# Kernel tuning notes

Measured on AMD Instinct MI355X. Metric: run time of the kernel, lower is better.

The kernel has to match this reference:

```python
import jax, jax.numpy as jnp
import numpy as np

OUT_SIZE = 7
SPATIAL_SCALE = 0.0625
SAMPLE_NUM = 2


def setup_inputs() -> dict:
    key = jax.random.key(0)
    k1, k2, k3, k4, k5, k6 = jax.random.split(key, 6)
    N, C, H, W = 4, 256, 96, 96
    K = 1024
    features = jax.random.normal(k1, (N, C, H, W), dtype=jnp.float32)
    img_h, img_w = H / SPATIAL_SCALE, W / SPATIAL_SCALE
    batch_idx = jax.random.randint(k2, (K,), 0, N).astype(jnp.float32)
    x1 = jax.random.uniform(k3, (K,)) * (img_w - 320.0)
    y1 = jax.random.uniform(k4, (K,)) * (img_h - 320.0)
    x2 = x1 + 16.0 + jax.random.uniform(k5, (K,)) * 300.0
    y2 = y1 + 16.0 + jax.random.uniform(k6, (K,)) * 300.0
    rois = jnp.stack([batch_idx, x1, y1, x2, y2], axis=1).astype(jnp.float32)
    return {"features": features, "rois": rois}


def _sample_coords(start, bin_size):
    # start, bin_size: [K]; returns [K, OUT_SIZE*SAMPLE_NUM] sample-point coords
    g = jnp.arange(OUT_SIZE * SAMPLE_NUM, dtype=jnp.float32)
    bin_idx = jnp.floor(g / SAMPLE_NUM)
    sub = g - bin_idx * SAMPLE_NUM
    offs = bin_idx + (sub + 0.5) / SAMPLE_NUM
    return start[:, None] + bin_size[:, None] * offs[None, :]


def _interp_1d(coord, size):
    # coord: [K, G] sample coords along one axis of a map of length `size`.
    valid = (coord >= -1.0) & (coord <= jnp.float32(size))
    c = jnp.clip(coord, 0.0, jnp.float32(size - 1))
    lo = jnp.floor(c)
    hi = jnp.minimum(lo + 1.0, jnp.float32(size - 1))
    frac = c - lo  # weight of hi; (1-frac) weight of lo
    return lo.astype(jnp.int32), hi.astype(jnp.int32), frac, valid


def roi_align(features, rois):
    N, C, H, W = features.shape
    b = rois[:, 0].astype(jnp.int32)
    x1, y1, x2, y2 = (rois[:, i] * SPATIAL_SCALE for i in (1, 2, 3, 4))
    roi_w = jnp.maximum(x2 - x1, 1.0)
    roi_h = jnp.maximum(y2 - y1, 1.0)
    bin_w = roi_w / OUT_SIZE
    bin_h = roi_h / OUT_SIZE

    ys = _sample_coords(y1, bin_h)  # [K, G]
    xs = _sample_coords(x1, bin_w)  # [K, G]
    ylo, yhi, fy, vy = _interp_1d(ys, H)
    xlo, xhi, fx, vx = _interp_1d(xs, W)

    bb = b[:, None, None]

    def gather(yi, xi):
        # -> [K, G, G, C]
        return features[bb, :, yi[:, :, None], xi[:, None, :]]

    wy_lo, wy_hi = (1.0 - fy), fy
    wx_lo, wx_hi = (1.0 - fx), fx

    def w2(wy, wx):
        return (wy[:, :, None] * wx[:, None, :])[..., None]

    val = (gather(ylo, xlo) * w2(wy_lo, wx_lo)
           + gather(ylo, xhi) * w2(wy_lo, wx_hi)
           + gather(yhi, xlo) * w2(wy_hi, wx_lo)
           + gather(yhi, xhi) * w2(wy_hi, wx_hi))
    mask = (vy[:, :, None] & vx[:, None, :])[..., None]
    val = jnp.where(mask, val, 0.0)

    K = rois.shape[0]
    G = OUT_SIZE * SAMPLE_NUM
    val = val.reshape(K, OUT_SIZE, SAMPLE_NUM, OUT_SIZE, SAMPLE_NUM, C)
    out = val.mean(axis=(2, 4))          # average the sample points per bin
    return jnp.transpose(out, (0, 3, 1, 2))  # [K, C, out, out]


def reference(features, rois):
    return roi_align(features, rois)
```

## Files before the change

### kernel.cpp

```cpp
#include <hip/hip_runtime.h>

#define CCH   256
#define FH    96
#define FW    96
#define HW    (FH*FW)
#define SCALE 0.0625f

#define HROWS 21
#define PSTR  28
#define PLANE (HROWS*PSTR)
#define WCH   32

__global__ __launch_bounds__(256, 8)
void roialign_kernel(const float* __restrict__ feat,
                     const float* __restrict__ rois,
                     float* __restrict__ out)
{
    __shared__ __align__(16) float win[4 * PLANE];
    __shared__ int   s_lo[2][14];
    __shared__ float s_wl[2][14], s_wh[2][14];

    const int k    = blockIdx.x >> 1;
    const int half = blockIdx.x & 1;
    const int tid  = threadIdx.x;
    const int w    = tid >> 6;
    const int ll   = tid & 63;

    const float x1 = rois[k*5+1] * SCALE;
    const float y1 = rois[k*5+2] * SCALE;
    const float x2 = rois[k*5+3] * SCALE;
    const float y2 = rois[k*5+4] * SCALE;
    const int   b  = (int)rois[k*5+0];
    const float binw = fmaxf(x2 - x1, 1.0f) * (1.0f/7.0f);
    const float binh = fmaxf(y2 - y1, 1.0f) * (1.0f/7.0f);

    if (tid < 28) {
        const int   axis  = (tid >= 14) ? 1 : 0;
        const int   g     = axis ? tid - 14 : tid;
        const float start = axis ? x1 : y1;
        const float bsz   = axis ? binw : binh;
        const float offs  = (float)(g >> 1) + 0.25f + 0.5f*(float)(g & 1);
        const float coord = start + bsz * offs;
        const bool  valid = (coord >= -1.0f) && (coord <= 96.0f);
        const float cc    = fminf(fmaxf(coord, 0.0f), 95.0f);
        const float lof   = floorf(cc);
        const float frac  = cc - lof;
        const float v     = valid ? 1.0f : 0.0f;
        s_lo[axis][g] = (int)lof;
        s_wl[axis][g] = (1.0f - frac) * v;
        s_wh[axis][g] = frac * v;
    }
    __syncthreads();

    const int row0 = s_lo[0][0];
    const int col0 = min(s_lo[1][0] & ~3, FW - 24);
    int hw_        = min(s_lo[0][13] + 1, FH-1) - row0 + 1;
    const int hwin = min(hw_, HROWS);
    const int nslot = hwin * 6;

    float* const wp = &win[w * PLANE];

    {
        const float4 z = make_float4(0.f, 0.f, 0.f, 0.f);
        #pragma unroll
        for (int j = 0; j < 3; ++j) {
            const int q = ll + 64*j;
            if (q < PLANE/4) *(float4*)&wp[q*4] = z;
        }
    }

    const bool active = ll < 49;
    const int  p  = active ? ll : 0;
    const int  oy = p / 7;
    const int  ox = p - oy*7;

    int   aL[4], aH[4];
    float w00[4], w01[4], w10[4], w11[4];
    #pragma unroll
    for (int sy = 0; sy < 2; ++sy) {
        const int   gy  = 2*oy + sy;
        const int   rlo = min(s_lo[0][gy] - row0,                 HROWS-1);
        const int   rhi = min(min(s_lo[0][gy]+1, FH-1) - row0,    HROWS-1);
        const float wyl = s_wl[0][gy], wyh = s_wh[0][gy];
        #pragma unroll
        for (int sx = 0; sx < 2; ++sx) {
            const int   gx  = 2*ox + sx;
            const int   clo = min(s_lo[1][gx] - col0, PSTR-2);
            const float wxl = s_wl[1][gx], wxh = s_wh[1][gx];
            const int   s   = sy*2 + sx;
            aL[s] = rlo*PSTR + clo;
            aH[s] = rhi*PSTR + clo;
            w00[s] = wyl*wxl*0.25f;  w01[s] = wyl*wxh*0.25f;
            w10[s] = wyh*wxl*0.25f;  w11[s] = wyh*wxh*0.25f;
        }
    }

    const int  sl1 = ll + 64;
    const int  r0  = ll  / 6, q0 = ll  - r0*6;
    const int  r1  = sl1 / 6, q1 = sl1 - r1*6;
    const bool L0  = ll  < nslot;
    const bool L1  = sl1 < nslot;
    const int  goff0 = min(row0 + r0, FH-1)*FW + col0 + q0*4;
    const int  goff1 = min(row0 + r1, FH-1)*FW + col0 + q1*4;
    const int  ld0   = min(r0, HROWS-1)*PSTR + q0*4;
    const int  ld1   = min(r1, HROWS-1)*PSTR + q1*4;

    const int    cb   = half*128 + w*WCH;
    const float* gch  = feat + (size_t)(b*CCH + cb) * HW;
    float*       outp = out  + ((size_t)k*CCH + cb)*49 + p;

    float4 st0, st1;
    if (L0) st0 = *(const float4*)(gch + goff0);
    if (L1) st1 = *(const float4*)(gch + goff1);

    for (int c = 0; c < WCH; ++c) {
        if (L0) *(float4*)&wp[ld0] = st0;
        if (L1) *(float4*)&wp[ld1] = st1;

        if (c + 1 < WCH) {
            const float* gn = gch + (size_t)(c+1)*HW;
            if (L0) st0 = *(const float4*)(gn + goff0);
            if (L1) st1 = *(const float4*)(gn + goff1);
        }

        if (active) {
            float acc = 0.0f;
            #pragma unroll
            for (int s = 0; s < 4; ++s) {
                acc += w00[s]*wp[aL[s]]   + w01[s]*wp[aL[s]+1]
                     + w10[s]*wp[aH[s]]   + w11[s]*wp[aH[s]+1];
            }
            outp[0] = acc;
        }
        outp += 49;
    }
}

extern "C" void kernel_launch(void* const* d_in, const int* in_sizes, int n_in,
                              void* d_out, int out_size, void* d_ws, size_t ws_size,
                              hipStream_t stream) {
    const float* feat = (const float*)d_in[0];
    const float* rois = (const float*)d_in[1];
    float*       outp = (float*)d_out;
    const int K = in_sizes[1] / 5;
    roialign_kernel<<<K*2, 256, 0, stream>>>(feat, rois, outp);
}
```

Before: 135.6 us.

## Apply y-interpolation while staging rows, making LDS hold per-sample-row vectors

Separates the bilinear interpolation: each loader thread reads the lo and hi feature rows for one y-sample and writes the y-blended row into shared memory. The compute threads then only perform the x-interpolation, with 8 LDS reads instead of 16 per output. The shared buffer becomes 14 sample rows instead of a 21-row window, at the cost of twice as many global loads per staged row, since adjacent samples' rows are fetched redundantly. Launch bounds occupancy hint is lowered from 8 to 6.

Measured after the change: 144.7 us. 6.7% more time.

```diff
diff --git a/kernel.cpp b/kernel.cpp
--- a/kernel.cpp
+++ b/kernel.cpp
@@ -6,19 +6,20 @@
 #define HW    (FH*FW)
 #define SCALE 0.0625f
 
-#define HROWS 21
-#define PSTR  28
-#define PLANE (HROWS*PSTR)
+#define G     14
+#define VSTR  28
+#define PLANE (G*VSTR)
 #define WCH   32
+#define NSLOT 84
 
-__global__ __launch_bounds__(256, 8)
+__global__ __launch_bounds__(256, 6)
 void roialign_kernel(const float* __restrict__ feat,
                      const float* __restrict__ rois,
                      float* __restrict__ out)
 {
-    __shared__ __align__(16) float win[4 * PLANE];
-    __shared__ int   s_lo[2][14];
-    __shared__ float s_wl[2][14], s_wh[2][14];
+    __shared__ __align__(16) float vbuf[4 * PLANE];
+    __shared__ int   s_lo[2][G];
+    __shared__ float s_wl[2][G], s_wh[2][G];
 
     const int k    = blockIdx.x >> 1;
     const int half = blockIdx.x & 1;
@@ -52,85 +53,81 @@
     }
     __syncthreads();
 
-    const int row0 = s_lo[0][0];
     const int col0 = min(s_lo[1][0] & ~3, FW - 24);
-    int hw_        = min(s_lo[0][13] + 1, FH-1) - row0 + 1;
-    const int hwin = min(hw_, HROWS);
-    const int nslot = hwin * 6;
-
-    float* const wp = &win[w * PLANE];
+    float* const wp = &vbuf[w * PLANE];
 
     {
         const float4 z = make_float4(0.f, 0.f, 0.f, 0.f);
-        #pragma unroll
-        for (int j = 0; j < 3; ++j) {
-            const int q = ll + 64*j;
-            if (q < PLANE/4) *(float4*)&wp[q*4] = z;
-        }
+        if (ll      < PLANE/4) *(float4*)&wp[ll*4]       = z;
+        if (ll + 64 < PLANE/4) *(float4*)&wp[(ll+64)*4]  = z;
     }
+
+    const int  gyA = ll / 6,  qA = ll - 6*gyA;
+    const int  sB  = ll + 64;
+    const bool LB  = sB < NSLOT;
+    const int  gyB = min(sB / 6, G-1);
+    const int  qB  = min(sB - 6*gyB, 5);
+    const float wylA = s_wl[0][gyA], wyhA = s_wh[0][gyA];
+    const float wylB = s_wl[0][gyB], wyhB = s_wh[0][gyB];
+    const int  rloA = s_lo[0][gyA], rhiA = min(rloA + 1, FH-1);
+    const int  rloB = s_lo[0][gyB], rhiB = min(rloB + 1, FH-1);
+    const int  goffAL = rloA*FW + col0 + 4*qA;
+    const int  goffAH = rhiA*FW + col0 + 4*qA;
+    const int  goffBL = rloB*FW + col0 + 4*qB;
+    const int  goffBH = rhiB*FW + col0 + 4*qB;
+    const int  ldA = gyA*VSTR + 4*qA;
+    const int  ldB = gyB*VSTR + 4*qB;
 
     const bool active = ll < 49;
     const int  p  = active ? ll : 0;
     const int  oy = p / 7;
     const int  ox = p - oy*7;
-
-    int   aL[4], aH[4];
-    float w00[4], w01[4], w10[4], w11[4];
-    #pragma unroll
-    for (int sy = 0; sy < 2; ++sy) {
-        const int   gy  = 2*oy + sy;
-        const int   rlo = min(s_lo[0][gy] - row0,                 HROWS-1);
-        const int   rhi = min(min(s_lo[0][gy]+1, FH-1) - row0,    HROWS-1);
-        const float wyl = s_wl[0][gy], wyh = s_wh[0][gy];
-        #pragma unroll
-        for (int sx = 0; sx < 2; ++sx) {
-            const int   gx  = 2*ox + sx;
-            const int   clo = min(s_lo[1][gx] - col0, PSTR-2);
-            const float wxl = s_wl[1][gx], wxh = s_wh[1][gx];
-            const int   s   = sy*2 + sx;
-            aL[s] = rlo*PSTR + clo;
-            aH[s] = rhi*PSTR + clo;
-            w00[s] = wyl*wxl*0.25f;  w01[s] = wyl*wxh*0.25f;
-            w10[s] = wyh*wxl*0.25f;  w11[s] = wyh*wxh*0.25f;
-        }
-    }
-
-    const int  sl1 = ll + 64;
-    const int  r0  = ll  / 6, q0 = ll  - r0*6;
-    const int  r1  = sl1 / 6, q1 = sl1 - r1*6;
-    const bool L0  = ll  < nslot;
-    const bool L1  = sl1 < nslot;
-    const int  goff0 = min(row0 + r0, FH-1)*FW + col0 + q0*4;
-    const int  goff1 = min(row0 + r1, FH-1)*FW + col0 + q1*4;
-    const int  ld0   = min(r0, HROWS-1)*PSTR + q0*4;
-    const int  ld1   = min(r1, HROWS-1)*PSTR + q1*4;
+    const int  gxA = 2*ox, gxB = 2*ox + 1;
+    const int  cloA = min(max(s_lo[1][gxA] - col0, 0), 23);
+    const int  cloB = min(max(s_lo[1][gxB] - col0, 0), 23);
+    const float wxlA = s_wl[1][gxA]*0.25f, wxhA = s_wh[1][gxA]*0.25f;
+    const float wxlB = s_wl[1][gxB]*0.25f, wxhB = s_wh[1][gxB]*0.25f;
+    const float* tpA = wp + (2*oy)*VSTR + cloA;
+    const float* tpB = wp + (2*oy)*VSTR + cloB;
 
     const int    cb   = half*128 + w*WCH;
     const float* gch  = feat + (size_t)(b*CCH + cb) * HW;
     float*       outp = out  + ((size_t)k*CCH + cb)*49 + p;
 
-    float4 st0, st1;
-    if (L0) st0 = *(const float4*)(gch + goff0);
-    if (L1) st1 = *(const float4*)(gch + goff1);
+    float4 aL, aH, bL, bH;
+    aL = *(const float4*)(gch + goffAL);
+    aH = *(const float4*)(gch + goffAH);
+    if (LB) { bL = *(const float4*)(gch + goffBL);
+              bH = *(const float4*)(gch + goffBH); }
 
     for (int c = 0; c < WCH; ++c) {
-        if (L0) *(float4*)&wp[ld0] = st0;
-        if (L1) *(float4*)&wp[ld1] = st1;
+        {
+            float4 v;
+            v.x = wylA*aL.x + wyhA*aH.x;  v.y = wylA*aL.y + wyhA*aH.y;
+            v.z = wylA*aL.z + wyhA*aH.z;  v.w = wylA*aL.w + wyhA*aH.w;
+            *(float4*)&wp[ldA] = v;
+        }
+        if (LB) {
+            float4 v;
+            v.x = wylB*bL.x + wyhB*bH.x;  v.y = wylB*bL.y + wyhB*bH.y;
+            v.z = wylB*bL.z + wyhB*bH.z;  v.w = wylB*bL.w + wyhB*bH.w;
+            *(float4*)&wp[ldB] = v;
+        }
 
         if (c + 1 < WCH) {
             const float* gn = gch + (size_t)(c+1)*HW;
-            if (L0) st0 = *(const float4*)(gn + goff0);
-            if (L1) st1 = *(const float4*)(gn + goff1);
+            aL = *(const float4*)(gn + goffAL);
+            aH = *(const float4*)(gn + goffAH);
+            if (LB) { bL = *(const float4*)(gn + goffBL);
+                      bH = *(const float4*)(gn + goffBH); }
         }
 
         if (active) {
-            float acc = 0.0f;
-            #pragma unroll
-            for (int s = 0; s < 4; ++s) {
-                acc += w00[s]*wp[aL[s]]   + w01[s]*wp[aL[s]+1]
-                     + w10[s]*wp[aH[s]]   + w11[s]*wp[aH[s]+1];
-            }
-            outp[0] = acc;
+            const float sA0 = tpA[0] + tpA[VSTR];
+            const float sA1 = tpA[1] + tpA[VSTR+1];
+            const float sB0 = tpB[0] + tpB[VSTR];
+            const float sB1 = tpB[1] + tpB[VSTR+1];
+            outp[0] = wxlA*sA0 + wxhA*sA1 + wxlB*sB0 + wxhB*sB1;
         }
         outp += 49;
     }
```
